# Kernel optimization log

Hardware: AMD Instinct MI355X
Metric: run time of the kernel (lower is better)

Reference implementation:

```python
import jax, jax.numpy as jnp
import numpy as np

B, T, K = 512, 512, 128
START, STOP = K - 2, K - 1
NEG = -10000.0


def setup_inputs() -> dict:
    key = jax.random.key(0)
    k1, k2, k3, k4 = jax.random.split(key, 4)
    feats = jax.random.normal(k1, (B, T, K), dtype=jnp.float32)
    transitions = jax.random.normal(k2, (K, K), dtype=jnp.float32)
    # CRF.__init__ clamps transitions INTO the start tag and OUT of the stop tag
    transitions = transitions.at[START, :].set(NEG).at[:, STOP].set(NEG)
    tags = jax.random.randint(k3, (B, T), 0, K - 2, dtype=jnp.int32)
    lengths = jax.random.randint(k4, (B,), 1, T + 1, dtype=jnp.int32)
    return {"feats": feats, "transitions": transitions, "tags": tags, "lengths": lengths}


def _forward_alg(feats, trans, lengths):
    # feats: [B, T, K]
    Bb, Tt, Kk = feats.shape
    alpha0 = jnp.full((Bb, Kk), NEG, dtype=feats.dtype).at[:, START].set(0.0)

    def step(alpha, emit):
        # tag_var[b, j, k] = emit[b, j] + trans[j, k] + alpha[b, k]
        tag_var = emit[:, :, None] + trans[None, :, :] + alpha[:, None, :]
        new = jax.nn.logsumexp(tag_var, axis=2)  # stable max + log-sum-exp
        return new, new

    _, alphas = jax.lax.scan(step, alpha0, jnp.swapaxes(feats, 0, 1))  # [T, B, K]
    alphas_all = jnp.concatenate([alpha0[None], alphas], axis=0)       # [T+1, B, K]
    # pick forward_var at position lengths[b] (original indexes [b, lens_[b], :])
    fv = alphas_all[lengths, jnp.arange(Bb)]                            # [B, K]
    terminal = fv + trans[STOP][None, :]
    return jax.nn.logsumexp(terminal, axis=1)                           # [B]


def _score_sentence(feats, trans, tags, lengths):
    Bb, Tt, Kk = feats.shape
    pos = jnp.arange(Tt)
    valid = pos[None, :] < lengths[:, None]                             # [B, T]
    # pad_stop_tags: tags with positions >= len replaced by STOP, then STOP appended
    tags_stop = jnp.where(valid, tags, STOP)
    pad_stop = jnp.concatenate(
        [tags_stop, jnp.full((Bb, 1), STOP, dtype=tags.dtype)], axis=1)  # [B, T+1]
    pad_start = jnp.concatenate(
        [jnp.full((Bb, 1), START, dtype=tags.dtype), tags], axis=1)     # [B, T+1]
    trans_terms = trans[pad_stop, pad_start]                            # [B, T+1]
    tmask = jnp.arange(Tt + 1)[None, :] <= lengths[:, None]             # i in [0, len]
    tscore = jnp.sum(jnp.where(tmask, trans_terms, 0.0), axis=1)
    emit = jnp.take_along_axis(feats, tags[:, :, None].astype(jnp.int32), axis=2)[:, :, 0]
    escore = jnp.sum(jnp.where(valid, emit, 0.0), axis=1)
    return tscore + escore                                              # [B]


def reference(feats, transitions, tags, lengths):
    forward_score = _forward_alg(feats, transitions, lengths)
    gold_score = _score_sentence(feats, transitions, tags, lengths)
    return jnp.mean(jnp.abs(forward_score - gold_score))
```

## Files before the change

### kernel.cpp

```cpp
#include <hip/hip_runtime.h>
#include <math.h>

#define KK 128
#define TT 512
#define BB 512
#define TAG_START 126
#define TAG_STOP 127

typedef float v4f __attribute__((ext_vector_type(4)));

#define XIDX(r) ((r) + (((r) >> 5) << 3))

__device__ __forceinline__ float quad_add(float x, int ctrl) {
    int yi;
    if (ctrl == 0xB1)
        yi = __builtin_amdgcn_update_dpp(0, __float_as_int(x), 0xB1, 0xF, 0xF, true);
    else
        yi = __builtin_amdgcn_update_dpp(0, __float_as_int(x), 0x4E, 0xF, 0xF, true);
    return x + __int_as_float(yi);
}

#define STEP_BARRIER() asm volatile("s_waitcnt lgkmcnt(0)\n\ts_barrier" ::: "memory")


__global__ __launch_bounds__(512) void order_kernel(const int* __restrict__ lengths,
                                                    int* __restrict__ order) {
    __shared__ int L[BB];
    int tid = threadIdx.x;
    L[tid] = lengths[tid];
    __syncthreads();
    int mylen = L[tid];
    int r = 0;
    for (int i = 0; i < BB; i++) {
        int li = L[i];
        r += (li > mylen) || (li == mylen && i < tid);
    }
    order[r] = tid;
}

__global__ __launch_bounds__(512, 4) void fused_kernel(
    const float* __restrict__ feats, const float* __restrict__ trans,
    const int* __restrict__ tags, const int* __restrict__ lengths,
    const int* __restrict__ order,
    float* __restrict__ fwd_out, float* __restrict__ gold_out) {
    int tid = threadIdx.x;

    if (blockIdx.x < BB) {
        int b = order[blockIdx.x];
        int w = tid >> 6;
        int l = tid & 63;
        int kq = l & 3;
        int row = 16 * w + (l >> 2);

        __shared__ __align__(16) float xs[2][160];
        __shared__ float As[2];
        __shared__ float redm[8], reds[8];

        const float* tp = trans + row * KK + 32 * kq;
        v4f tv[8];
#pragma unroll
        for (int q = 0; q < 8; q++) {
            asm volatile("global_load_dwordx4 %0, %1, off"
                         : "=v"(tv[q]) : "v"(tp + 4 * q));
        }
        int len = lengths[b];
        const float* fbr = feats + (size_t)b * TT * KK + row;
        asm volatile("s_waitcnt vmcnt(0)"
                     : "+v"(tv[0]), "+v"(tv[1]), "+v"(tv[2]), "+v"(tv[3]),
                       "+v"(tv[4]), "+v"(tv[5]), "+v"(tv[6]), "+v"(tv[7]));

        float m32 = -1e30f;
#pragma unroll
        for (int q = 0; q < 8; q++)
            m32 = fmaxf(m32, fmaxf(fmaxf(tv[q].x, tv[q].y), fmaxf(tv[q].z, tv[q].w)));
        m32 = fmaxf(m32, __shfl_xor(m32, 1));
        float Mj = fmaxf(m32, __shfl_xor(m32, 2));

        float Erow[32];
#pragma unroll
        for (int q = 0; q < 8; q++) {
            Erow[4 * q + 0] = __expf(tv[q].x - Mj);
            Erow[4 * q + 1] = __expf(tv[q].y - Mj);
            Erow[4 * q + 2] = __expf(tv[q].z - Mj);
            Erow[4 * q + 3] = __expf(tv[q].w - Mj);
        }

        if (kq == 0) xs[0][XIDX(row)] = (row == TAG_START) ? 1.0f : 0.0f;
        if (tid == 0) { As[0] = 0.f; As[1] = 0.f; }

        float alpha = 0.f, A = 0.f;
        float emb[8];
#pragma unroll
        for (int d = 0; d < 8; d++) {
            int tf = (d < len) ? d : (len - 1);
            emb[d] = fbr[(size_t)tf * KK];
        }
        __syncthreads();

        int tmax = (len + 7) & ~7;
        for (int t0 = 0; t0 < tmax; t0 += 8) {
#pragma unroll
            for (int d = 0; d < 8; d++) {
                int t = t0 + d;
                if (t < len) {
                    float em = emb[d];
                    int tf = (t + 8 < len) ? (t + 8) : (len - 1);
                    emb[d] = fbr[(size_t)tf * KK];

                    int cur = t & 1, nxt = cur ^ 1;
                    float Sn = As[nxt];
                    float fac = __expf(em + Mj + A - Sn);
                    const v4f* x4 = (const v4f*)(xs[cur] + 40 * kq);
                    float s0 = 0.f, s1 = 0.f, s2 = 0.f, s3 = 0.f;
#pragma unroll
                    for (int q = 0; q < 8; q++) {
                        v4f xv = x4[q];
                        s0 = fmaf(Erow[4 * q + 0], xv.x, s0);
                        s1 = fmaf(Erow[4 * q + 1], xv.y, s1);
                        s2 = fmaf(Erow[4 * q + 2], xv.z, s2);
                        s3 = fmaf(Erow[4 * q + 3], xv.w, s3);
                    }
                    float yq = (s0 + s1) + (s2 + s3);
                    yq = quad_add(yq, 0xB1);
                    float y = quad_add(yq, 0x4E);
                    if (kq == 0) xs[nxt][XIDX(row)] = y * fac;
                    alpha = em + Mj + A + __logf(y);
                    if (tid == 0) As[cur] = alpha;
                    A = Sn;
                    STEP_BARRIER();
                }
            }
        }

        float term = (kq == 0) ? (alpha + trans[TAG_STOP * KK + row]) : -1e30f;
        float m = term;
#pragma unroll
        for (int off = 32; off >= 1; off >>= 1) m = fmaxf(m, __shfl_xor(m, off));
        float s = (kq == 0) ? __expf(term - m) : 0.f;
#pragma unroll
        for (int off = 32; off >= 1; off >>= 1) s += __shfl_xor(s, off);
        if (l == 0) { redm[w] = m; reds[w] = s; }
        __syncthreads();
        if (tid == 0) {
            float M2 = redm[0];
            for (int i = 1; i < 8; i++) M2 = fmaxf(M2, redm[i]);
            float S2 = 0.f;
            for (int i = 0; i < 8; i++) S2 += reds[i] * __expf(redm[i] - M2);
            fwd_out[b] = M2 + __logf(S2);
        }
    } else {
        int b = blockIdx.x - BB;
        int len = lengths[b];
        const int* tg = tags + (size_t)b * TT;
        const float* fb = feats + (size_t)b * TT * KK;
        float acc = 0.f;
        for (int i = tid; i <= len; i += 512) {
            int from = (i == 0) ? TAG_START : tg[i - 1];
            int to = (i < len) ? tg[i] : TAG_STOP;
            acc += trans[to * KK + from];
        }
        for (int t = tid; t < len; t += 512)
            acc += fb[(size_t)t * KK + tg[t]];
        __shared__ float sred[8];
#pragma unroll
        for (int off = 32; off >= 1; off >>= 1) acc += __shfl_xor(acc, off);
        if ((tid & 63) == 0) sred[tid >> 6] = acc;
        __syncthreads();
        if (tid == 0) {
            float s = 0.f;
            for (int i = 0; i < 8; i++) s += sred[i];
            gold_out[b] = s;
        }
    }
}

__global__ __launch_bounds__(512) void final_kernel(const float* __restrict__ fwd_s,
                                                    const float* __restrict__ gold_s,
                                                    float* __restrict__ out) {
    int tid = threadIdx.x;
    float v = fabsf(fwd_s[tid] - gold_s[tid]);
#pragma unroll
    for (int off = 32; off >= 1; off >>= 1) v += __shfl_xor(v, off);
    __shared__ float sred[8];
    if ((tid & 63) == 0) sred[tid >> 6] = v;
    __syncthreads();
    if (tid == 0) {
        float s = 0.f;
        for (int i = 0; i < 8; i++) s += sred[i];
        out[0] = s / (float)BB;
    }
}

extern "C" void kernel_launch(void* const* d_in, const int* in_sizes, int n_in,
                              void* d_out, int out_size, void* d_ws, size_t ws_size,
                              hipStream_t stream) {
    const float* feats = (const float*)d_in[0];
    const float* trans = (const float*)d_in[1];
    const int* tags = (const int*)d_in[2];
    const int* lengths = (const int*)d_in[3];

    float* ws = (float*)d_ws;
    float* fwdv = ws;
    float* goldv = ws + BB;
    int* order = (int*)(ws + 2 * BB);

    order_kernel<<<1, 512, 0, stream>>>(lengths, order);
    fused_kernel<<<2 * BB, 512, 0, stream>>>(feats, trans, tags, lengths, order,
                                             fwdv, goldv);
    final_kernel<<<1, 512, 0, stream>>>(fwdv, goldv, (float*)d_out);
}
```

Before: 361.4 us.

## Remap matvec lanes to 4 rows x 8 columns with DPP transpose-reduce

Changes the per-step matrix-vector partition so each lane holds 8 columns of 4 transition rows instead of 32 columns of one row. Each step then reads 8 floats of the alpha vector from LDS per lane instead of 32, and the four partial sums are combined with a DPP butterfly transpose-reduce across 16 lanes. The aim is to cut LDS read traffic and latency on the serial per-timestep critical path. In exchange it adds more cross-lane DPP and select operations per step, and it changes the LDS padding layout.

```diff
diff --git a/kernel.cpp b/kernel.cpp
--- a/kernel.cpp
+++ b/kernel.cpp
@@ -9,15 +9,12 @@
 
 typedef float v4f __attribute__((ext_vector_type(4)));
 
-#define XIDX(r) ((r) + (((r) >> 5) << 3))
-
-__device__ __forceinline__ float quad_add(float x, int ctrl) {
-    int yi;
-    if (ctrl == 0xB1)
-        yi = __builtin_amdgcn_update_dpp(0, __float_as_int(x), 0xB1, 0xF, 0xF, true);
-    else
-        yi = __builtin_amdgcn_update_dpp(0, __float_as_int(x), 0x4E, 0xF, 0xF, true);
-    return x + __int_as_float(yi);
+#define XI(j) ((j) + (((j) >> 5) << 2))
+
+template <int CTRL>
+__device__ __forceinline__ float dpp_movf(float x) {
+    return __int_as_float(
+        __builtin_amdgcn_update_dpp(0, __float_as_int(x), CTRL, 0xF, 0xF, true));
 }
 
 #define STEP_BARRIER() asm volatile("s_waitcnt lgkmcnt(0)\n\ts_barrier" ::: "memory")
@@ -44,48 +41,72 @@
     const int* __restrict__ order,
     float* __restrict__ fwd_out, float* __restrict__ gold_out) {
     int tid = threadIdx.x;
+    int w = tid >> 6;
+    int l = tid & 63;
 
     if (blockIdx.x < BB) {
         int b = order[blockIdx.x];
-        int w = tid >> 6;
-        int l = tid & 63;
-        int kq = l & 3;
-        int row = 16 * w + (l >> 2);
 
         __shared__ __align__(16) float xs[2][160];
         __shared__ float As[2];
         __shared__ float redm[8], reds[8];
 
-        const float* tp = trans + row * KK + 32 * kq;
+        int g = (l >> 4) & 3;
+        int c = l & 15;
+        bool b0 = (l & 1) != 0;
+        bool b1 = (l & 2) != 0;
+        int row_mine = 16 * w + 4 * g + 2 * (l & 1) + ((l >> 1) & 1);
+        int xoff = 8 * c + 4 * (c >> 2);
+        int xw = XI(row_mine);
+        bool writer = (l & 12) == 0;
+
         v4f tv[8];
 #pragma unroll
-        for (int q = 0; q < 8; q++) {
+        for (int r = 0; r < 4; r++) {
+            const float* tp = trans + (16 * w + 4 * g + r) * KK + 8 * c;
             asm volatile("global_load_dwordx4 %0, %1, off"
-                         : "=v"(tv[q]) : "v"(tp + 4 * q));
+                         : "=v"(tv[2 * r]) : "v"(tp));
+            asm volatile("global_load_dwordx4 %0, %1, off"
+                         : "=v"(tv[2 * r + 1]) : "v"(tp + 4));
         }
         int len = lengths[b];
-        const float* fbr = feats + (size_t)b * TT * KK + row;
+        const float* fbr = feats + (size_t)b * TT * KK + row_mine;
         asm volatile("s_waitcnt vmcnt(0)"
                      : "+v"(tv[0]), "+v"(tv[1]), "+v"(tv[2]), "+v"(tv[3]),
                        "+v"(tv[4]), "+v"(tv[5]), "+v"(tv[6]), "+v"(tv[7]));
 
-        float m32 = -1e30f;
-#pragma unroll
-        for (int q = 0; q < 8; q++)
-            m32 = fmaxf(m32, fmaxf(fmaxf(tv[q].x, tv[q].y), fmaxf(tv[q].z, tv[q].w)));
-        m32 = fmaxf(m32, __shfl_xor(m32, 1));
-        float Mj = fmaxf(m32, __shfl_xor(m32, 2));
+        float Mj0, Mj1, Mj2, Mj3;
+        {
+            float m[4];
+#pragma unroll
+            for (int r = 0; r < 4; r++) {
+                v4f aL = tv[2 * r], aH = tv[2 * r + 1];
+                float mm = fmaxf(fmaxf(fmaxf(aL.x, aL.y), fmaxf(aL.z, aL.w)),
+                                 fmaxf(fmaxf(aH.x, aH.y), fmaxf(aH.z, aH.w)));
+#pragma unroll
+                for (int off = 1; off <= 8; off <<= 1)
+                    mm = fmaxf(mm, __shfl_xor(mm, off));
+                m[r] = mm;
+            }
+            Mj0 = m[0]; Mj1 = m[1]; Mj2 = m[2]; Mj3 = m[3];
+        }
+        float Mj_mine = b0 ? (b1 ? Mj3 : Mj2) : (b1 ? Mj1 : Mj0);
 
         float Erow[32];
 #pragma unroll
-        for (int q = 0; q < 8; q++) {
-            Erow[4 * q + 0] = __expf(tv[q].x - Mj);
-            Erow[4 * q + 1] = __expf(tv[q].y - Mj);
-            Erow[4 * q + 2] = __expf(tv[q].z - Mj);
-            Erow[4 * q + 3] = __expf(tv[q].w - Mj);
-        }
-
-        if (kq == 0) xs[0][XIDX(row)] = (row == TAG_START) ? 1.0f : 0.0f;
+        for (int r = 0; r < 4; r++) {
+            float mr = (r == 0) ? Mj0 : (r == 1) ? Mj1 : (r == 2) ? Mj2 : Mj3;
+            Erow[8 * r + 0] = __expf(tv[2 * r].x - mr);
+            Erow[8 * r + 1] = __expf(tv[2 * r].y - mr);
+            Erow[8 * r + 2] = __expf(tv[2 * r].z - mr);
+            Erow[8 * r + 3] = __expf(tv[2 * r].w - mr);
+            Erow[8 * r + 4] = __expf(tv[2 * r + 1].x - mr);
+            Erow[8 * r + 5] = __expf(tv[2 * r + 1].y - mr);
+            Erow[8 * r + 6] = __expf(tv[2 * r + 1].z - mr);
+            Erow[8 * r + 7] = __expf(tv[2 * r + 1].w - mr);
+        }
+
+        if (writer) xs[0][xw] = (row_mine == TAG_START) ? 1.0f : 0.0f;
         if (tid == 0) { As[0] = 0.f; As[1] = 0.f; }
 
         float alpha = 0.f, A = 0.f;
@@ -109,22 +130,39 @@
 
                     int cur = t & 1, nxt = cur ^ 1;
                     float Sn = As[nxt];
-                    float fac = __expf(em + Mj + A - Sn);
-                    const v4f* x4 = (const v4f*)(xs[cur] + 40 * kq);
-                    float s0 = 0.f, s1 = 0.f, s2 = 0.f, s3 = 0.f;
-#pragma unroll
-                    for (int q = 0; q < 8; q++) {
-                        v4f xv = x4[q];
-                        s0 = fmaf(Erow[4 * q + 0], xv.x, s0);
-                        s1 = fmaf(Erow[4 * q + 1], xv.y, s1);
-                        s2 = fmaf(Erow[4 * q + 2], xv.z, s2);
-                        s3 = fmaf(Erow[4 * q + 3], xv.w, s3);
-                    }
-                    float yq = (s0 + s1) + (s2 + s3);
-                    yq = quad_add(yq, 0xB1);
-                    float y = quad_add(yq, 0x4E);
-                    if (kq == 0) xs[nxt][XIDX(row)] = y * fac;
-                    alpha = em + Mj + A + __logf(y);
+                    float fac = __expf(em + Mj_mine + A - Sn);
+                    const v4f* xp = (const v4f*)(xs[cur] + xoff);
+                    v4f xa = xp[0], xb = xp[1];
+                    float a0 = 0.f, a1 = 0.f, a2 = 0.f, a3 = 0.f;
+                    a0 = fmaf(Erow[0], xa.x, a0);  a0 = fmaf(Erow[1], xa.y, a0);
+                    a0 = fmaf(Erow[2], xa.z, a0);  a0 = fmaf(Erow[3], xa.w, a0);
+                    a0 = fmaf(Erow[4], xb.x, a0);  a0 = fmaf(Erow[5], xb.y, a0);
+                    a0 = fmaf(Erow[6], xb.z, a0);  a0 = fmaf(Erow[7], xb.w, a0);
+                    a1 = fmaf(Erow[8], xa.x, a1);  a1 = fmaf(Erow[9], xa.y, a1);
+                    a1 = fmaf(Erow[10], xa.z, a1); a1 = fmaf(Erow[11], xa.w, a1);
+                    a1 = fmaf(Erow[12], xb.x, a1); a1 = fmaf(Erow[13], xb.y, a1);
+                    a1 = fmaf(Erow[14], xb.z, a1); a1 = fmaf(Erow[15], xb.w, a1);
+                    a2 = fmaf(Erow[16], xa.x, a2); a2 = fmaf(Erow[17], xa.y, a2);
+                    a2 = fmaf(Erow[18], xa.z, a2); a2 = fmaf(Erow[19], xa.w, a2);
+                    a2 = fmaf(Erow[20], xb.x, a2); a2 = fmaf(Erow[21], xb.y, a2);
+                    a2 = fmaf(Erow[22], xb.z, a2); a2 = fmaf(Erow[23], xb.w, a2);
+                    a3 = fmaf(Erow[24], xa.x, a3); a3 = fmaf(Erow[25], xa.y, a3);
+                    a3 = fmaf(Erow[26], xa.z, a3); a3 = fmaf(Erow[27], xa.w, a3);
+                    a3 = fmaf(Erow[28], xb.x, a3); a3 = fmaf(Erow[29], xb.y, a3);
+                    a3 = fmaf(Erow[30], xb.z, a3); a3 = fmaf(Erow[31], xb.w, a3);
+                    float k0 = b0 ? a2 : a0;
+                    float k1 = b0 ? a3 : a1;
+                    float s0 = b0 ? a0 : a2;
+                    float s1 = b0 ? a1 : a3;
+                    k0 += dpp_movf<0xB1>(s0);
+                    k1 += dpp_movf<0xB1>(s1);
+                    float kk = b1 ? k1 : k0;
+                    float ss = b1 ? k0 : k1;
+                    kk += dpp_movf<0x4E>(ss);
+                    kk += dpp_movf<0x124>(kk);
+                    kk += dpp_movf<0x128>(kk);
+                    if (writer) xs[nxt][xw] = kk * fac;
+                    alpha = em + Mj_mine + A + __logf(kk);
                     if (tid == 0) As[cur] = alpha;
                     A = Sn;
                     STEP_BARRIER();
@@ -132,11 +170,11 @@
             }
         }
 
-        float term = (kq == 0) ? (alpha + trans[TAG_STOP * KK + row]) : -1e30f;
+        float term = writer ? (alpha + trans[TAG_STOP * KK + row_mine]) : -1e30f;
         float m = term;
 #pragma unroll
         for (int off = 32; off >= 1; off >>= 1) m = fmaxf(m, __shfl_xor(m, off));
-        float s = (kq == 0) ? __expf(term - m) : 0.f;
+        float s = writer ? __expf(term - m) : 0.f;
 #pragma unroll
         for (int off = 32; off >= 1; off >>= 1) s += __shfl_xor(s, off);
         if (l == 0) { redm[w] = m; reds[w] = s; }
```

Result: faster. 341.1 us (-5.6%).

## Split CRF forward recursion into concurrent forward and backward halves meeting midway

Applied to the files above, without the earlier changes.

Each block now runs the forward alpha recursion over the first half of the sequence on four waves and a backward beta recursion over the second half on the other four waves, then combines them with a logsumexp at the meeting point. This roughly halves the number of serial barrier-separated steps per sequence. Each thread also now holds an 8x8 tile of exp(transitions) and reduces partial sums across 16 lanes with DPP shuffles instead of a 32-wide row slice per quad. In exchange it uses more registers (64 per-thread transition values) and adds a transposed strided load for the backward tile.

```diff
diff --git a/kernel.cpp b/kernel.cpp
--- a/kernel.cpp
+++ b/kernel.cpp
@@ -8,16 +8,14 @@
 #define TAG_STOP 127
 
 typedef float v4f __attribute__((ext_vector_type(4)));
-
-#define XIDX(r) ((r) + (((r) >> 5) << 3))
-
-__device__ __forceinline__ float quad_add(float x, int ctrl) {
-    int yi;
-    if (ctrl == 0xB1)
-        yi = __builtin_amdgcn_update_dpp(0, __float_as_int(x), 0xB1, 0xF, 0xF, true);
-    else
-        yi = __builtin_amdgcn_update_dpp(0, __float_as_int(x), 0x4E, 0xF, 0xF, true);
-    return x + __int_as_float(yi);
+typedef float v2f __attribute__((ext_vector_type(2)));
+
+#define XI(j) ((j) + (((j) >> 5) << 2))
+
+template <int CTRL>
+__device__ __forceinline__ float dpp_movf(float x) {
+    return __int_as_float(
+        __builtin_amdgcn_update_dpp(0, __float_as_int(x), CTRL, 0xF, 0xF, true));
 }
 
 #define STEP_BARRIER() asm volatile("s_waitcnt lgkmcnt(0)\n\ts_barrier" ::: "memory")
@@ -44,102 +42,266 @@
     const int* __restrict__ order,
     float* __restrict__ fwd_out, float* __restrict__ gold_out) {
     int tid = threadIdx.x;
+    int w = tid >> 6;
+    int l = tid & 63;
 
     if (blockIdx.x < BB) {
         int b = order[blockIdx.x];
-        int w = tid >> 6;
-        int l = tid & 63;
-        int kq = l & 3;
-        int row = 16 * w + (l >> 2);
-
-        __shared__ __align__(16) float xs[2][160];
-        __shared__ float As[2];
+        int len = lengths[b];
+        int m = len >> 1;
+        int nb = len - m;
+
+        __shared__ __align__(16) float xsf[2][160];
+        __shared__ __align__(16) float xsb[2][160];
+        __shared__ float Asf[2], Asb[2];
+        __shared__ float sh_a[KK], sh_b[KK];
         __shared__ float redm[8], reds[8];
 
-        const float* tp = trans + row * KK + 32 * kq;
-        v4f tv[8];
-#pragma unroll
-        for (int q = 0; q < 8; q++) {
-            asm volatile("global_load_dwordx4 %0, %1, off"
-                         : "=v"(tv[q]) : "v"(tp + 4 * q));
-        }
-        int len = lengths[b];
-        const float* fbr = feats + (size_t)b * TT * KK + row;
-        asm volatile("s_waitcnt vmcnt(0)"
-                     : "+v"(tv[0]), "+v"(tv[1]), "+v"(tv[2]), "+v"(tv[3]),
-                       "+v"(tv[4]), "+v"(tv[5]), "+v"(tv[6]), "+v"(tv[7]));
-
-        float m32 = -1e30f;
-#pragma unroll
-        for (int q = 0; q < 8; q++)
-            m32 = fmaxf(m32, fmaxf(fmaxf(tv[q].x, tv[q].y), fmaxf(tv[q].z, tv[q].w)));
-        m32 = fmaxf(m32, __shfl_xor(m32, 1));
-        float Mj = fmaxf(m32, __shfl_xor(m32, 2));
-
-        float Erow[32];
-#pragma unroll
-        for (int q = 0; q < 8; q++) {
-            Erow[4 * q + 0] = __expf(tv[q].x - Mj);
-            Erow[4 * q + 1] = __expf(tv[q].y - Mj);
-            Erow[4 * q + 2] = __expf(tv[q].z - Mj);
-            Erow[4 * q + 3] = __expf(tv[q].w - Mj);
-        }
-
-        if (kq == 0) xs[0][XIDX(row)] = (row == TAG_START) ? 1.0f : 0.0f;
-        if (tid == 0) { As[0] = 0.f; As[1] = 0.f; }
-
-        float alpha = 0.f, A = 0.f;
-        float emb[8];
-#pragma unroll
-        for (int d = 0; d < 8; d++) {
-            int tf = (d < len) ? d : (len - 1);
-            emb[d] = fbr[(size_t)tf * KK];
-        }
+        bool is_fwd = (w < 4);
+        int wg = w & 3;
+        int g = (l >> 4) & 3;
+        int c = l & 15;
+        bool b0 = (l & 1) != 0;
+        bool b1 = (l & 2) != 0;
+        int base = 32 * wg + 8 * g;
+        int rA = base + (b0 ? 4 : 0) + (b1 ? 2 : 0);
+        int xoff = 8 * c + 4 * (c >> 2);
+        bool writer = (l & 12) == 0;
+
+        float Ef[64];
+        if (is_fwd) {
+#pragma unroll
+            for (int r = 0; r < 8; r++) {
+                v4f lo = *(const v4f*)(trans + (base + r) * KK + 8 * c);
+                v4f hi = *(const v4f*)(trans + (base + r) * KK + 8 * c + 4);
+                Ef[8 * r + 0] = lo.x; Ef[8 * r + 1] = lo.y;
+                Ef[8 * r + 2] = lo.z; Ef[8 * r + 3] = lo.w;
+                Ef[8 * r + 4] = hi.x; Ef[8 * r + 5] = hi.y;
+                Ef[8 * r + 6] = hi.z; Ef[8 * r + 7] = hi.w;
+            }
+        } else {
+#pragma unroll
+            for (int r = 0; r < 8; r++)
+#pragma unroll
+                for (int cc = 0; cc < 8; cc++)
+                    Ef[8 * r + cc] = trans[(8 * c + cc) * KK + (base + r)];
+        }
+        float Mj[8];
+#pragma unroll
+        for (int r = 0; r < 8; r++) {
+            float mm = Ef[8 * r];
+#pragma unroll
+            for (int j = 1; j < 8; j++) mm = fmaxf(mm, Ef[8 * r + j]);
+#pragma unroll
+            for (int off = 1; off <= 8; off <<= 1)
+                mm = fmaxf(mm, __shfl_xor(mm, off));
+            Mj[r] = mm;
+        }
+#pragma unroll
+        for (int r = 0; r < 8; r++)
+#pragma unroll
+            for (int j = 0; j < 8; j++)
+                Ef[8 * r + j] = __expf(Ef[8 * r + j] - Mj[r]);
+        float MjA = b0 ? (b1 ? Mj[6] : Mj[4]) : (b1 ? Mj[2] : Mj[0]);
+        float MjB = b0 ? (b1 ? Mj[7] : Mj[5]) : (b1 ? Mj[3] : Mj[1]);
+
+        const float* fA = feats + (size_t)b * TT * KK + rA;
+        const float* fB = fA + 1;
+        float embA[4], embB[4];
+        float emIA = 0.f, emIB = 0.f;
+        if (is_fwd) {
+            int mm1 = (m > 0) ? (m - 1) : 0;
+#pragma unroll
+            for (int d = 0; d < 4; d++) {
+                int tf = (d < m) ? d : mm1;
+                embA[d] = fA[(size_t)tf * KK];
+                embB[d] = fB[(size_t)tf * KK];
+            }
+        } else {
+            emIA = fA[(size_t)(len - 1) * KK];
+            emIB = fB[(size_t)(len - 1) * KK];
+#pragma unroll
+            for (int d = 0; d < 4; d++) {
+                int t = len - 2 - d;
+                if (t < 0) t = 0;
+                embA[d] = fA[(size_t)t * KK];
+                embB[d] = fB[(size_t)t * KK];
+            }
+        }
+
+        float alphaA, alphaB;
+        if (is_fwd) {
+            alphaA = (rA == TAG_START) ? 0.f : -1e30f;
+            alphaB = (rA + 1 == TAG_START) ? 0.f : -1e30f;
+        } else {
+            alphaA = -1e30f; alphaB = -1e30f;
+        }
+
+        if (is_fwd) {
+            if (writer) {
+                v2f x0;
+                x0.x = (rA == TAG_START) ? 1.f : 0.f;
+                x0.y = (rA + 1 == TAG_START) ? 1.f : 0.f;
+                *(v2f*)&xsf[0][XI(rA)] = x0;
+            }
+            if (tid == 0) { Asf[0] = 0.f; Asf[1] = 0.f; }
+        } else {
+            if (writer) {
+                v2f x0;
+                x0.x = __expf(trans[TAG_STOP * KK + rA] + emIA);
+                x0.y = __expf(trans[TAG_STOP * KK + rA + 1] + emIB);
+                *(v2f*)&xsb[0][XI(rA)] = x0;
+            }
+            if (tid == 256) { Asb[0] = 0.f; Asb[1] = 0.f; }
+        }
+        float A = 0.f;
         __syncthreads();
 
-        int tmax = (len + 7) & ~7;
-        for (int t0 = 0; t0 < tmax; t0 += 8) {
-#pragma unroll
-            for (int d = 0; d < 8; d++) {
-                int t = t0 + d;
-                if (t < len) {
-                    float em = emb[d];
-                    int tf = (t + 8 < len) ? (t + 8) : (len - 1);
-                    emb[d] = fbr[(size_t)tf * KK];
-
-                    int cur = t & 1, nxt = cur ^ 1;
-                    float Sn = As[nxt];
-                    float fac = __expf(em + Mj + A - Sn);
-                    const v4f* x4 = (const v4f*)(xs[cur] + 40 * kq);
-                    float s0 = 0.f, s1 = 0.f, s2 = 0.f, s3 = 0.f;
-#pragma unroll
-                    for (int q = 0; q < 8; q++) {
-                        v4f xv = x4[q];
-                        s0 = fmaf(Erow[4 * q + 0], xv.x, s0);
-                        s1 = fmaf(Erow[4 * q + 1], xv.y, s1);
-                        s2 = fmaf(Erow[4 * q + 2], xv.z, s2);
-                        s3 = fmaf(Erow[4 * q + 3], xv.w, s3);
+        for (int i0 = 0; i0 < nb; i0 += 4) {
+#pragma unroll
+            for (int d = 0; d < 4; d++) {
+                int i = i0 + d;
+                if (i < nb) {
+                    if (is_fwd) {
+                        if (i < m) {
+                            float emA = embA[d], emB = embB[d];
+                            int tf = (i + 4 < m) ? (i + 4) : (m - 1);
+                            embA[d] = fA[(size_t)tf * KK];
+                            embB[d] = fB[(size_t)tf * KK];
+
+                            int cur = i & 1, nxt = cur ^ 1;
+                            float Sn = Asf[nxt];
+                            float facA = __expf(emA + MjA + A - Sn);
+                            float facB = __expf(emB + MjB + A - Sn);
+                            const v4f* xp = (const v4f*)(xsf[cur] + xoff);
+                            v4f xa = xp[0], xb = xp[1];
+                            float acc[8];
+#pragma unroll
+                            for (int r = 0; r < 8; r++) {
+                                float a = 0.f;
+                                a = fmaf(Ef[8 * r + 0], xa.x, a);
+                                a = fmaf(Ef[8 * r + 1], xa.y, a);
+                                a = fmaf(Ef[8 * r + 2], xa.z, a);
+                                a = fmaf(Ef[8 * r + 3], xa.w, a);
+                                a = fmaf(Ef[8 * r + 4], xb.x, a);
+                                a = fmaf(Ef[8 * r + 5], xb.y, a);
+                                a = fmaf(Ef[8 * r + 6], xb.z, a);
+                                a = fmaf(Ef[8 * r + 7], xb.w, a);
+                                acc[r] = a;
+                            }
+                            float k4[4];
+#pragma unroll
+                            for (int ii = 0; ii < 4; ii++) {
+                                float kp = b0 ? acc[ii + 4] : acc[ii];
+                                float sp = b0 ? acc[ii] : acc[ii + 4];
+                                k4[ii] = kp + dpp_movf<0xB1>(sp);
+                            }
+                            float k0, k1;
+                            {
+                                float kp = b1 ? k4[2] : k4[0];
+                                float sp = b1 ? k4[0] : k4[2];
+                                k0 = kp + dpp_movf<0x4E>(sp);
+                            }
+                            {
+                                float kp = b1 ? k4[3] : k4[1];
+                                float sp = b1 ? k4[1] : k4[3];
+                                k1 = kp + dpp_movf<0x4E>(sp);
+                            }
+                            k0 += dpp_movf<0x124>(k0);
+                            k0 += dpp_movf<0x128>(k0);
+                            k1 += dpp_movf<0x124>(k1);
+                            k1 += dpp_movf<0x128>(k1);
+                            if (writer) {
+                                v2f xn; xn.x = k0 * facA; xn.y = k1 * facB;
+                                *(v2f*)&xsf[nxt][XI(rA)] = xn;
+                            }
+                            if (tid == 0) Asf[cur] = emA + MjA + A + __logf(k0);
+                            if (i == m - 1) {
+                                alphaA = emA + MjA + A + __logf(k0);
+                                alphaB = emB + MjB + A + __logf(k1);
+                            }
+                            A = Sn;
+                        }
+                    } else {
+                        float emNA = embA[d];
+                        float emNB = embB[d];
+                        {
+                            int tp = len - 6 - i;
+                            if (tp < 0) tp = 0;
+                            embA[d] = fA[(size_t)tp * KK];
+                            embB[d] = fB[(size_t)tp * KK];
+                        }
+                        int cur = i & 1, nxt = cur ^ 1;
+                        float Sn = Asb[nxt];
+                        float facA = __expf(emNA + MjA + A - Sn);
+                        float facB = __expf(emNB + MjB + A - Sn);
+                        const v4f* xp = (const v4f*)(xsb[cur] + xoff);
+                        v4f xa = xp[0], xb = xp[1];
+                        float acc[8];
+#pragma unroll
+                        for (int r = 0; r < 8; r++) {
+                            float a = 0.f;
+                            a = fmaf(Ef[8 * r + 0], xa.x, a);
+                            a = fmaf(Ef[8 * r + 1], xa.y, a);
+                            a = fmaf(Ef[8 * r + 2], xa.z, a);
+                            a = fmaf(Ef[8 * r + 3], xa.w, a);
+                            a = fmaf(Ef[8 * r + 4], xb.x, a);
+                            a = fmaf(Ef[8 * r + 5], xb.y, a);
+                            a = fmaf(Ef[8 * r + 6], xb.z, a);
+                            a = fmaf(Ef[8 * r + 7], xb.w, a);
+                            acc[r] = a;
+                        }
+                        float k4[4];
+#pragma unroll
+                        for (int ii = 0; ii < 4; ii++) {
+                            float kp = b0 ? acc[ii + 4] : acc[ii];
+                            float sp = b0 ? acc[ii] : acc[ii + 4];
+                            k4[ii] = kp + dpp_movf<0xB1>(sp);
+                        }
+                        float k0, k1;
+                        {
+                            float kp = b1 ? k4[2] : k4[0];
+                            float sp = b1 ? k4[0] : k4[2];
+                            k0 = kp + dpp_movf<0x4E>(sp);
+                        }
+                        {
+                            float kp = b1 ? k4[3] : k4[1];
+                            float sp = b1 ? k4[1] : k4[3];
+                            k1 = kp + dpp_movf<0x4E>(sp);
+                        }
+                        k0 += dpp_movf<0x124>(k0);
+                        k0 += dpp_movf<0x128>(k0);
+                        k1 += dpp_movf<0x124>(k1);
+                        k1 += dpp_movf<0x128>(k1);
+                        if (writer) {
+                            v2f xn; xn.x = k0 * facA; xn.y = k1 * facB;
+                            *(v2f*)&xsb[nxt][XI(rA)] = xn;
+                        }
+                        if (tid == 256) Asb[cur] = MjA + A + __logf(k0);
+                        if (i == nb - 1) {
+                            alphaA = MjA + A + __logf(k0);
+                            alphaB = MjB + A + __logf(k1);
+                        }
+                        A = Sn;
                     }
-                    float yq = (s0 + s1) + (s2 + s3);
-                    yq = quad_add(yq, 0xB1);
-                    float y = quad_add(yq, 0x4E);
-                    if (kq == 0) xs[nxt][XIDX(row)] = y * fac;
-                    alpha = em + Mj + A + __logf(y);
-                    if (tid == 0) As[cur] = alpha;
-                    A = Sn;
                     STEP_BARRIER();
                 }
             }
         }
 
-        float term = (kq == 0) ? (alpha + trans[TAG_STOP * KK + row]) : -1e30f;
-        float m = term;
-#pragma unroll
-        for (int off = 32; off >= 1; off >>= 1) m = fmaxf(m, __shfl_xor(m, off));
-        float s = (kq == 0) ? __expf(term - m) : 0.f;
+        if (writer) {
+            if (is_fwd) { sh_a[rA] = alphaA; sh_a[rA + 1] = alphaB; }
+            else        { sh_b[rA] = alphaA; sh_b[rA + 1] = alphaB; }
+        }
+        __syncthreads();
+        float term = (tid < KK) ? (sh_a[tid] + sh_b[tid]) : -1e30f;
+        float mx = term;
+#pragma unroll
+        for (int off = 32; off >= 1; off >>= 1) mx = fmaxf(mx, __shfl_xor(mx, off));
+        float s = (tid < KK) ? __expf(term - mx) : 0.f;
 #pragma unroll
         for (int off = 32; off >= 1; off >>= 1) s += __shfl_xor(s, off);
-        if (l == 0) { redm[w] = m; reds[w] = s; }
+        if (l == 0) { redm[w] = mx; reds[w] = s; }
         __syncthreads();
         if (tid == 0) {
             float M2 = redm[0];
```

Measured after the change: 316.6 us. -12.4%, faster.
